# Kernel optimization log

Hardware: AMD Instinct MI355X
Metric: run time of the kernel (lower is better)

Reference implementation:

```python
import jax, jax.numpy as jnp
import numpy as np


def setup_inputs() -> dict:
    key = jax.random.key(0)
    k1, k2, k3 = jax.random.split(key, 3)
    B, L, J, C = 2048, 20, 25, 256  # batch, seq (fixed to 20 by kernel shape), joints, channels
    F, K = 64, 4                    # filters, hops
    x = jax.random.normal(k1, (B, L, J, C), dtype=jnp.float32)
    A = jax.random.uniform(k2, (J, J), dtype=jnp.float32)
    kernel = jax.random.normal(k3, (F, K, L), dtype=jnp.float32) * 0.1
    return {"x": x, "A": A, "kernel": kernel}


def reference(x, A, kernel):
    # Faithful to source: tf.pow(A, k) is ELEMENTWISE power (A**0 = ones matrix).
    hops = kernel.shape[1]
    # [K, J, J] elementwise powers of A, computed once (source recomputes per filter/step)
    Apow = A[None, :, :] ** jnp.arange(hops, dtype=A.dtype)[:, None, None]
    # Output per timestep l is sum over filters n of sum over hops k of
    # kernel[n,k,l] * (A**k @ x[:,l]); the filter sum factors out:
    w = kernel.sum(axis=0)  # [K, L]
    # Source returns a python list over l of [B, J, C]; we stack -> [L, B, J, C]
    out = jnp.einsum('kl,kij,bljc->lbic', w, Apow, x)
    return out
```

## Files before the change

kernel.cpp:

```cpp
#include <hip/hip_runtime.h>

#define BB   2048
#define LL   20
#define JJ   25
#define CC   256
#define FF   64
#define KK   4
#define JPAD 28

__global__ __launch_bounds__(256) void GCNLayer_72602127172024_kernel(
    const float* __restrict__ x,
    const float* __restrict__ A,
    const float* __restrict__ kern,
    float* __restrict__ out)
{
    __shared__ float w_sh[KK];
    __shared__ float Ms[JJ * JPAD];

    const int tid = threadIdx.x;
    const int gid = blockIdx.x;
    const int l   = gid >> 9;
    const int bb  = (gid & 511) << 2;

    {
        const int k    = tid >> 6;
        const int lane = tid & 63;
        float v = kern[lane * (KK * LL) + k * LL + l];
        v += __shfl_xor(v, 32, 64);
        v += __shfl_xor(v, 16, 64);
        v += __shfl_xor(v, 8, 64);
        v += __shfl_xor(v, 4, 64);
        v += __shfl_xor(v, 2, 64);
        v += __shfl_xor(v, 1, 64);
        if (lane == 0) w_sh[k] = v;
    }
    __syncthreads();

    const float w0 = w_sh[0], w1 = w_sh[1], w2 = w_sh[2], w3 = w_sh[3];

    for (int e = tid; e < JJ * JPAD; e += 256) {
        const int i = e / JPAD;
        const int j = e - i * JPAD;
        float m = 0.0f;
        if (j < JJ) {
            const float a = A[i * JJ + j];
            m = w0 + a * (w1 + a * (w2 + a * w3));
        }
        Ms[e] = m;
    }
    __syncthreads();

    const int bsub = tid >> 6;
    const int c4   = tid & 63;
    const int b    = bb + bsub;

    const float4* __restrict__ xin =
        reinterpret_cast<const float4*>(x) + ((b * LL + l) * JJ) * 64 + c4;
    float4* __restrict__ oout =
        reinterpret_cast<float4*>(out) + ((l * BB + b) * JJ) * 64 + c4;

    float4 xv[JJ];
#pragma unroll
    for (int j = 0; j < JJ; ++j) xv[j] = xin[j * 64];

#pragma unroll
    for (int i = 0; i < JJ; ++i) {
        const float4* mrow = reinterpret_cast<const float4*>(Ms + i * JPAD);
        float4 acc;
        acc.x = 0.0f; acc.y = 0.0f; acc.z = 0.0f; acc.w = 0.0f;
#pragma unroll
        for (int j4 = 0; j4 < 7; ++j4) {
            const float4 m4 = mrow[j4];
#pragma unroll
            for (int comp = 0; comp < 4; ++comp) {
                const int j = j4 * 4 + comp;
                if (j < JJ) {
                    const float m = (comp == 0) ? m4.x : (comp == 1) ? m4.y
                                   : (comp == 2) ? m4.z : m4.w;
                    acc.x = fmaf(m, xv[j].x, acc.x);
                    acc.y = fmaf(m, xv[j].y, acc.y);
                    acc.z = fmaf(m, xv[j].z, acc.z);
                    acc.w = fmaf(m, xv[j].w, acc.w);
                }
            }
        }
        oout[i * 64] = acc;
    }
}

extern "C" void kernel_launch(void* const* d_in, const int* in_sizes, int n_in,
                              void* d_out, int out_size, void* d_ws, size_t ws_size,
                              hipStream_t stream) {
    const float* x    = (const float*)d_in[0];
    const float* A    = (const float*)d_in[1];
    const float* kern = (const float*)d_in[2];
    float* out        = (float*)d_out;

    const int grid = LL * (BB / 4);
    GCNLayer_72602127172024_kernel<<<grid, 256, 0, stream>>>(x, A, kern, out);
}
```

Before: 419.7 us.

## Precompute per-timestep mixing matrix in separate kernel and stream x with nontemporal ops

Moves the per-timestep hop-weighted matrix construction into a small precompute kernel that writes a transposed, padded matrix to workspace. The main kernel no longer runs a kernel-weight reduction or shared-memory setup per block; it reads matrix entries from global memory, which should be uniform across the block and cacheable. The loop is reordered to an outer-product form with 25 accumulators, and x loads and output stores use nontemporal hints. This adds a second launch and relies on the workspace, and the main kernel is memory-bound, so the gain may be limited.

```diff
diff --git a/kernel.cpp b/kernel.cpp
--- a/kernel.cpp
+++ b/kernel.cpp
@@ -6,25 +6,22 @@
 #define CC   256
 #define FF   64
 #define KK   4
-#define JPAD 28
+#define IPAD 32
+#define MTSZ (JJ * IPAD)
 
-__global__ __launch_bounds__(256) void GCNLayer_72602127172024_kernel(
-    const float* __restrict__ x,
+typedef float f4 __attribute__((ext_vector_type(4)));
+
+__global__ __launch_bounds__(256) void GCN_precompute_Mt(
     const float* __restrict__ A,
     const float* __restrict__ kern,
-    float* __restrict__ out)
+    float* __restrict__ Mt)
 {
+    const int l = blockIdx.x;
     __shared__ float w_sh[KK];
-    __shared__ float Ms[JJ * JPAD];
-
-    const int tid = threadIdx.x;
-    const int gid = blockIdx.x;
-    const int l   = gid >> 9;
-    const int bb  = (gid & 511) << 2;
 
     {
-        const int k    = tid >> 6;
-        const int lane = tid & 63;
+        const int k    = threadIdx.x >> 6;
+        const int lane = threadIdx.x & 63;
         float v = kern[lane * (KK * LL) + k * LL + l];
         v += __shfl_xor(v, 32, 64);
         v += __shfl_xor(v, 16, 64);
@@ -38,54 +35,60 @@
 
     const float w0 = w_sh[0], w1 = w_sh[1], w2 = w_sh[2], w3 = w_sh[3];
 
-    for (int e = tid; e < JJ * JPAD; e += 256) {
-        const int i = e / JPAD;
-        const int j = e - i * JPAD;
+    for (int e = threadIdx.x; e < MTSZ; e += 256) {
+        const int j = e / IPAD;
+        const int i = e - j * IPAD;
         float m = 0.0f;
-        if (j < JJ) {
+        if (i < JJ) {
             const float a = A[i * JJ + j];
             m = w0 + a * (w1 + a * (w2 + a * w3));
         }
-        Ms[e] = m;
+        Mt[l * MTSZ + e] = m;
     }
-    __syncthreads();
+}
+
+__global__ __launch_bounds__(256, 4) void GCNLayer_72602127172024_kernel(
+    const float* __restrict__ x,
+    const float* __restrict__ Mt,
+    float* __restrict__ out)
+{
+    const int tid = threadIdx.x;
+    const int gid = blockIdx.x;
+    const int l   = gid >> 9;
+    const int bb  = (gid & 511) << 2;
 
     const int bsub = tid >> 6;
     const int c4   = tid & 63;
     const int b    = bb + bsub;
 
-    const float4* __restrict__ xin =
-        reinterpret_cast<const float4*>(x) + ((b * LL + l) * JJ) * 64 + c4;
-    float4* __restrict__ oout =
-        reinterpret_cast<float4*>(out) + ((l * BB + b) * JJ) * 64 + c4;
+    const f4* __restrict__ xin =
+        reinterpret_cast<const f4*>(x) + ((b * LL + l) * JJ) * 64 + c4;
+    f4* __restrict__ oout =
+        reinterpret_cast<f4*>(out) + ((l * BB + b) * JJ) * 64 + c4;
 
-    float4 xv[JJ];
+    const float* __restrict__ Mtl = Mt + l * MTSZ;
+
+    f4 acc[JJ];
 #pragma unroll
-    for (int j = 0; j < JJ; ++j) xv[j] = xin[j * 64];
+    for (int i = 0; i < JJ; ++i) acc[i] = (f4){0.0f, 0.0f, 0.0f, 0.0f};
 
 #pragma unroll
-    for (int i = 0; i < JJ; ++i) {
-        const float4* mrow = reinterpret_cast<const float4*>(Ms + i * JPAD);
-        float4 acc;
-        acc.x = 0.0f; acc.y = 0.0f; acc.z = 0.0f; acc.w = 0.0f;
+    for (int j = 0; j < JJ; ++j) {
+        const f4 xj = __builtin_nontemporal_load(xin + j * 64);
+        const float* __restrict__ mcol = Mtl + j * IPAD;
 #pragma unroll
-        for (int j4 = 0; j4 < 7; ++j4) {
-            const float4 m4 = mrow[j4];
+        for (int i = 0; i < JJ; ++i) {
+            const float m = mcol[i];
+            acc[i].x = fmaf(m, xj.x, acc[i].x);
+            acc[i].y = fmaf(m, xj.y, acc[i].y);
+            acc[i].z = fmaf(m, xj.z, acc[i].z);
+            acc[i].w = fmaf(m, xj.w, acc[i].w);
+        }
+    }
+
 #pragma unroll
-            for (int comp = 0; comp < 4; ++comp) {
-                const int j = j4 * 4 + comp;
-                if (j < JJ) {
-                    const float m = (comp == 0) ? m4.x : (comp == 1) ? m4.y
-                                   : (comp == 2) ? m4.z : m4.w;
-                    acc.x = fmaf(m, xv[j].x, acc.x);
-                    acc.y = fmaf(m, xv[j].y, acc.y);
-                    acc.z = fmaf(m, xv[j].z, acc.z);
-                    acc.w = fmaf(m, xv[j].w, acc.w);
-                }
-            }
-        }
-        oout[i * 64] = acc;
-    }
+    for (int i = 0; i < JJ; ++i)
+        __builtin_nontemporal_store(acc[i], oout + i * 64);
 }
 
 extern "C" void kernel_launch(void* const* d_in, const int* in_sizes, int n_in,
@@ -95,7 +98,10 @@
     const float* A    = (const float*)d_in[1];
     const float* kern = (const float*)d_in[2];
     float* out        = (float*)d_out;
+    float* Mt         = (float*)d_ws;
+
+    GCN_precompute_Mt<<<LL, 256, 0, stream>>>(A, kern, Mt);
 
     const int grid = LL * (BB / 4);
-    GCNLayer_72602127172024_kernel<<<grid, 256, 0, stream>>>(x, A, kern, out);
+    GCNLayer_72602127172024_kernel<<<grid, 256, 0, stream>>>(x, Mt, out);
 }
```

New measurement: 530.5 us. 1.26x slower.
